# Kernel optimization log

Hardware: AMD Instinct MI355X
Metric: run time of the kernel (lower is better)

## Reference

```python
import jax
import jax.numpy as jnp
from jax import lax
import numpy as np

L, B, D_IN, D = 1024, 16, 2048, 2048
K = 3  # n_in == n_out -> k = 3, highway uses x directly


def setup_inputs() -> dict:
    key = jax.random.key(0)
    k1, k2 = jax.random.split(key)
    x = jax.random.normal(k1, (L, B, D_IN), dtype=jnp.float32)
    c0 = jnp.zeros((B, D), dtype=jnp.float32)
    # learned params: projection weight (n_in, n_out*k) and bias (2*n_out)
    weight = jax.random.normal(k2, (D_IN, D * K), dtype=jnp.float32) * (1.0 / np.sqrt(D_IN))
    bias = jnp.zeros((2 * D,), dtype=jnp.float32)
    return {"x": x, "c0": c0, "weight": weight, "bias": bias}


def reference(x, c0, weight, bias):
    # x: [L, B, n_in], c0: [B, d], weight: [n_in, d*3], bias: [2*d]
    Llen, Bsz, _ = x.shape
    d = c0.shape[-1]
    u = jnp.einsum("lbi,ik->lbk", x, weight).reshape(Llen, Bsz, d, K)
    u0 = u[..., 0]                                   # candidate
    g1 = jax.nn.sigmoid(u[..., 1] + bias[:d])        # forget gate
    g2 = jax.nn.sigmoid(u[..., 2] + bias[d:])        # highway/reset gate

    # sequential recurrence: c_t = (c_{t-1} - u0_t) * g1_t + u0_t
    def step(c_prev, inp):
        u0_t, g1_t = inp
        c_t = (c_prev - u0_t) * g1_t + u0_t
        return c_t, c_t

    c_last, cs = lax.scan(step, c0, (u0, g1))
    # h_t = (tanh(c_t) - x_t) * g2_t + x_t   (use_tanh=1, k=3 highway on x)
    h = (jnp.tanh(cs) - x) * g2 + x
    return h, c_last
```

## Files before the change

### kernel.cpp

```cpp
#include <hip/hip_runtime.h>
#include <hip/hip_bf16.h>
#include <cstdint>

#define L_SEQ 1024
#define BSZ   16
#define DIN   2048
#define DD    2048
#define MROWS (L_SEQ * BSZ)
#define NCOLS (3 * DD)
#define BKT   64
#define NT    (DIN / BKT)

typedef __attribute__((ext_vector_type(8))) short  short8;
typedef __attribute__((ext_vector_type(4))) float  f32x4;
typedef __attribute__((ext_vector_type(4))) ushort ushort4v;

typedef const __attribute__((address_space(1))) void* gas_ptr;
typedef __attribute__((address_space(3))) void*       las_ptr;

#define GLOAD16(g, l) __builtin_amdgcn_global_load_lds((gas_ptr)(g), (las_ptr)(l), 16, 0, 0)

__device__ __forceinline__ float bf2f(ushort u) {
    return __uint_as_float(((uint32_t)u) << 16);
}
__device__ __forceinline__ ushort f2bf(float f) {
    uint32_t u = __float_as_uint(f);
    uint32_t r = u + 0x7FFFu + ((u >> 16) & 1u);
    return (ushort)(r >> 16);
}

__global__ __launch_bounds__(256) void cvt_x_kernel(const f32x4* __restrict__ x,
                                                    ushort4v* __restrict__ xb, int n4) {
    int i = blockIdx.x * blockDim.x + threadIdx.x;
    int stride = gridDim.x * blockDim.x;
    for (; i < n4; i += stride) {
        f32x4 v = x[i];
        ushort4v o;
        o.x = f2bf(v.x); o.y = f2bf(v.y); o.z = f2bf(v.z); o.w = f2bf(v.w);
        xb[i] = o;
    }
}

__global__ __launch_bounds__(256) void transpose_w_kernel(const float* __restrict__ W,
                                                          ushort* __restrict__ WT) {
    __shared__ float tile[64][65];
    int k0 = blockIdx.x * 64;
    int n0 = blockIdx.y * 64;
    int c  = threadIdx.x & 63;
    int r0 = threadIdx.x >> 6;
#pragma unroll
    for (int rr = 0; rr < 16; ++rr) {
        int r = r0 + rr * 4;
        tile[r][c] = W[(size_t)(k0 + r) * NCOLS + n0 + c];
    }
    __syncthreads();
#pragma unroll
    for (int rr = 0; rr < 16; ++rr) {
        int r = r0 + rr * 4;
        int n = n0 + r;
        int nprime = (n % 3) * DD + (n / 3);
        WT[(size_t)nprime * DIN + k0 + c] = f2bf(tile[c][r]);
    }
}

#define SLOT(b, s) (&lds8[(((b) << 2) + (s)) * 8192])

#define STAGE_A(b, h, kt) do {                                                   \
    const ushort* _g = Ab + (size_t)((h) * 64 + idx) * DIN + (kt) * BKT + akc;   \
    ushort* _l = SLOT(b, (h)) + tid * 8;                                         \
    GLOAD16(_g, _l);                                                             \
    GLOAD16(_g + (size_t)128 * DIN, _l + 4096);                                  \
} while (0)

#define STAGE_B(b, h2, kt) do {                                                  \
    const ushort* _g0 = Bb + (size_t)(brow0 + (h2) * 32) * DIN + (kt) * BKT + akc;\
    const ushort* _g1 = Bb + (size_t)(brow1 + (h2) * 32) * DIN + (kt) * BKT + akc;\
    ushort* _l = SLOT(b, 2 + (h2)) + tid * 8;                                    \
    GLOAD16(_g0, _l);                                                            \
    GLOAD16(_g1, _l + 4096);                                                     \
} while (0)

#define LD_A(b, h) do { const ushort* _s = SLOT(b, (h)) + a_rb;                  \
    _Pragma("unroll") for (int _m = 0; _m < 4; ++_m) {                           \
        aF[_m][0] = *(const short8*)(_s + _m * 1024 + cs0);                      \
        aF[_m][1] = *(const short8*)(_s + _m * 1024 + cs1); }                    \
} while (0)

#define LD_B(b, h2, bF) do { const ushort* _s = SLOT(b, 2 + (h2)) + b_rb;        \
    _Pragma("unroll") for (int _n = 0; _n < 2; ++_n) {                           \
        bF[_n][0] = *(const short8*)(_s + _n * 1024 + cs0);                      \
        bF[_n][1] = *(const short8*)(_s + _n * 1024 + cs1); }                    \
} while (0)

#define MM(mb, bF, nb) do {                                                      \
    __builtin_amdgcn_s_setprio(1);                                               \
    _Pragma("unroll") for (int _m = 0; _m < 4; ++_m)                             \
    _Pragma("unroll") for (int _n = 0; _n < 2; ++_n) {                           \
        acc[(mb)+_m][(nb)+_n] = __builtin_amdgcn_mfma_f32_16x16x32_bf16(         \
            aF[_m][0], bF[_n][0], acc[(mb)+_m][(nb)+_n], 0, 0, 0);               \
        acc[(mb)+_m][(nb)+_n] = __builtin_amdgcn_mfma_f32_16x16x32_bf16(         \
            aF[_m][1], bF[_n][1], acc[(mb)+_m][(nb)+_n], 0, 0, 0); }             \
    __builtin_amdgcn_s_setprio(0);                                               \
    __builtin_amdgcn_sched_barrier(0);                                           \
} while (0)

#define BAR() __builtin_amdgcn_s_barrier()

__global__ __launch_bounds__(512, 2) void sru_gemm8(const ushort* __restrict__ A,
                                                    const ushort* __restrict__ Bt,
                                                    const float*  __restrict__ bias,
                                                    ushort* __restrict__ u0,
                                                    ushort* __restrict__ g1,
                                                    ushort* __restrict__ g2) {
    __shared__ alignas(16) ushort lds8[65536];

    int bid = blockIdx.x;
    int swz = (bid & 7) * 192 + (bid >> 3);
    int bm0 = (swz / 24) * 256;
    int bn0 = (swz % 24) * 256;

    int tid  = threadIdx.x;
    int wave = tid >> 6, lane = tid & 63;
    int wm = wave >> 2, wn = wave & 3;

    int idx    = tid >> 3;
    int schunk = (tid & 7) ^ (idx & 7);
    int akc    = schunk * 8;
    int brow0  = (idx >> 5) * 64 + (idx & 31);
    int brow1  = ((idx >> 5) + 2) * 64 + (idx & 31);
    const ushort* Ab = A  + (size_t)bm0 * DIN;
    const ushort* Bb = Bt + (size_t)bn0 * DIN;

    int lrow = lane & 15, lk = lane >> 4, lx = lane & 7;
    int cs0  = ((0 + lk) ^ lx) * 8;
    int cs1  = ((4 + lk) ^ lx) * 8;
    int a_rb = (wm * 64 + lrow) * 64;
    int b_rb = (wn * 32 + lrow) * 64;

    f32x4 acc[8][4];
    f32x4 zero = {0.f, 0.f, 0.f, 0.f};
#pragma unroll
    for (int i = 0; i < 8; ++i)
#pragma unroll
        for (int j = 0; j < 4; ++j) acc[i][j] = zero;

    STAGE_A(0, 0, 0); STAGE_A(0, 1, 0); STAGE_B(0, 0, 0); STAGE_B(0, 1, 0);
    STAGE_A(1, 0, 1); STAGE_B(1, 0, 1);
    asm volatile("s_waitcnt vmcnt(4)" ::: "memory");
    BAR();

    short8 aF[4][2], bF0[2][2], bF1[2][2];

    for (int t = 0; t < NT; ++t) {
        int cur = t & 1, nxt = cur ^ 1;
        int kt1 = (t + 1 < NT) ? t + 1 : NT - 1;
        int kt2 = (t + 2 < NT) ? t + 2 : NT - 1;
        LD_A(cur, 0); LD_B(cur, 0, bF0);
        STAGE_A(nxt, 1, kt1);
        BAR(); MM(0, bF0, 0); BAR();
        LD_B(cur, 1, bF1);
        STAGE_B(nxt, 1, kt1);
        BAR(); MM(0, bF1, 2); BAR();
        LD_A(cur, 1);
        STAGE_A(cur, 0, kt2);
        BAR(); MM(4, bF0, 0); BAR();
        STAGE_B(cur, 0, kt2);
        asm volatile("s_waitcnt vmcnt(4)" ::: "memory");
        BAR(); MM(4, bF1, 2); BAR();
    }
    asm volatile("s_waitcnt vmcnt(0)" ::: "memory");

    int region = bn0 >> 11;
    int col_l  = (bn0 & (DD - 1)) + wn * 64 + (lane & 15);
#pragma unroll
    for (int mf = 0; mf < 8; ++mf) {
        int rowb = bm0 + wm * 128 + mf * 16 + ((lane >> 4) << 2);
#pragma unroll
        for (int nf = 0; nf < 4; ++nf) {
            int col = col_l + nf * 16;
#pragma unroll
            for (int r = 0; r < 4; ++r) {
                float v = acc[mf][nf][r];
                size_t o = (size_t)(rowb + r) * DD + col;
                if (region == 0) {
                    u0[o] = f2bf(v);
                } else {
                    float z = v + bias[(region - 1) * DD + col];
                    float g = 1.f / (1.f + __expf(-z));
                    (region == 1 ? g1 : g2)[o] = f2bf(g);
                }
            }
        }
    }
}

__global__ __launch_bounds__(64) void sru_rec(const ushort* __restrict__ u0,
                                              const ushort* __restrict__ g1,
                                              const ushort* __restrict__ g2,
                                              const float*  __restrict__ x,
                                              const float*  __restrict__ c0,
                                              float* __restrict__ h,
                                              float* __restrict__ c_last) {
    int t = blockIdx.x * 64 + threadIdx.x;
    float c = c0[t];
#pragma unroll 8
    for (int l = 0; l < L_SEQ; ++l) {
        int ix = l * (BSZ * DD) + t;
        float uu  = bf2f(u0[ix]);
        float gg1 = bf2f(g1[ix]);
        float gg2 = bf2f(g2[ix]);
        float xx  = x[ix];
        c = (c - uu) * gg1 + uu;
        float e  = __expf(-2.f * fabsf(c));
        float th = (1.f - e) / (1.f + e);
        th = copysignf(th, c);
        h[ix] = (th - xx) * gg2 + xx;
    }
    c_last[t] = c;
}

extern "C" void kernel_launch(void* const* d_in, const int* in_sizes, int n_in,
                              void* d_out, int out_size, void* d_ws, size_t ws_size,
                              hipStream_t stream) {
    const float* x    = (const float*)d_in[0];
    const float* c0   = (const float*)d_in[1];
    const float* W    = (const float*)d_in[2];
    const float* bias = (const float*)d_in[3];
    float* out = (float*)d_out;

    char* ws = (char*)d_ws;
    ushort* xb = (ushort*)(ws);
    ushort* WT = (ushort*)(ws + 67108864);
    ushort* u0 = (ushort*)(ws + 92274688);
    ushort* g1 = (ushort*)(ws + 159383552);
    ushort* g2 = (ushort*)(ws + 226492416);

    hipLaunchKernelGGL(cvt_x_kernel, dim3(2048), dim3(256), 0, stream,
                       (const f32x4*)x, (ushort4v*)xb, MROWS * DIN / 4);
    hipLaunchKernelGGL(transpose_w_kernel, dim3(32, 96), dim3(256), 0, stream, W, WT);
    hipLaunchKernelGGL(sru_gemm8, dim3(1536), dim3(512), 0, stream, xb, WT, bias, u0, g1, g2);
    hipLaunchKernelGGL(sru_rec, dim3(512), dim3(64), 0, stream,
                       u0, g1, g2, x, c0, out, out + (size_t)MROWS * DD);
}
```

Before: 630.2 us.

## Transpose MFMA output layout for packed bf16 epilogue stores and read bf16 x

Swaps the MFMA operand order so each lane's accumulator holds four consecutive columns instead of four rows. The epilogue can then pack values with v_cvt_pk_bf16_f32 and write 8-byte stores rather than scattered 2-byte ones, and the bias is loaded as a float4. The recurrence kernel now reads the bf16 copy of x instead of the fp32 input, which halves that stream's traffic. The cost is that the highway term uses x rounded to bf16, so h loses some precision.

```diff
diff --git a/kernel.cpp b/kernel.cpp
--- a/kernel.cpp
+++ b/kernel.cpp
@@ -97,9 +97,9 @@
     _Pragma("unroll") for (int _m = 0; _m < 4; ++_m)                             \
     _Pragma("unroll") for (int _n = 0; _n < 2; ++_n) {                           \
         acc[(mb)+_m][(nb)+_n] = __builtin_amdgcn_mfma_f32_16x16x32_bf16(         \
-            aF[_m][0], bF[_n][0], acc[(mb)+_m][(nb)+_n], 0, 0, 0);               \
+            bF[_n][0], aF[_m][0], acc[(mb)+_m][(nb)+_n], 0, 0, 0);               \
         acc[(mb)+_m][(nb)+_n] = __builtin_amdgcn_mfma_f32_16x16x32_bf16(         \
-            aF[_m][1], bF[_n][1], acc[(mb)+_m][(nb)+_n], 0, 0, 0); }             \
+            bF[_n][1], aF[_m][1], acc[(mb)+_m][(nb)+_n], 0, 0, 0); }             \
     __builtin_amdgcn_s_setprio(0);                                               \
     __builtin_amdgcn_sched_barrier(0);                                           \
 } while (0)
@@ -171,24 +171,44 @@
     asm volatile("s_waitcnt vmcnt(0)" ::: "memory");
 
     int region = bn0 >> 11;
-    int col_l  = (bn0 & (DD - 1)) + wn * 64 + (lane & 15);
-#pragma unroll
-    for (int mf = 0; mf < 8; ++mf) {
-        int rowb = bm0 + wm * 128 + mf * 16 + ((lane >> 4) << 2);
-#pragma unroll
-        for (int nf = 0; nf < 4; ++nf) {
-            int col = col_l + nf * 16;
-#pragma unroll
-            for (int r = 0; r < 4; ++r) {
-                float v = acc[mf][nf][r];
-                size_t o = (size_t)(rowb + r) * DD + col;
-                if (region == 0) {
-                    u0[o] = f2bf(v);
-                } else {
-                    float z = v + bias[(region - 1) * DD + col];
-                    float g = 1.f / (1.f + __expf(-z));
-                    (region == 1 ? g1 : g2)[o] = f2bf(g);
-                }
+    int colb = (bn0 & (DD - 1)) + wn * 64 + ((lane >> 4) << 2);
+    int rowm = bm0 + wm * 128 + (lane & 15);
+    if (region == 0) {
+#pragma unroll
+        for (int j = 0; j < 4; ++j)
+#pragma unroll
+            for (int i = 0; i < 4; ++i) {
+                f32x4 v = acc[i][j];
+                uint32_t lo, hi;
+                asm("v_cvt_pk_bf16_f32 %0, %1, %2" : "=v"(lo) : "v"(v[0]), "v"(v[1]));
+                asm("v_cvt_pk_bf16_f32 %0, %1, %2" : "=v"(hi) : "v"(v[2]), "v"(v[3]));
+                uint2 pk; pk.x = lo; pk.y = hi;
+                *(uint2*)&u0[(size_t)(rowm + i * 16) * DD + colb + j * 16] = pk;
+                f32x4 w = acc[4 + i][j];
+                asm("v_cvt_pk_bf16_f32 %0, %1, %2" : "=v"(lo) : "v"(w[0]), "v"(w[1]));
+                asm("v_cvt_pk_bf16_f32 %0, %1, %2" : "=v"(hi) : "v"(w[2]), "v"(w[3]));
+                pk.x = lo; pk.y = hi;
+                *(uint2*)&u0[(size_t)(rowm + 64 + i * 16) * DD + colb + j * 16] = pk;
+            }
+    } else {
+        const float* bp = bias + (size_t)(region - 1) * DD;
+        ushort* gp = (region == 1) ? g1 : g2;
+#pragma unroll
+        for (int j = 0; j < 4; ++j) {
+            float4 bv = *(const float4*)&bp[colb + j * 16];
+#pragma unroll
+            for (int i = 0; i < 8; ++i) {
+                f32x4 v = acc[i][j];
+                float s0 = 1.f / (1.f + __expf(-(v[0] + bv.x)));
+                float s1 = 1.f / (1.f + __expf(-(v[1] + bv.y)));
+                float s2 = 1.f / (1.f + __expf(-(v[2] + bv.z)));
+                float s3 = 1.f / (1.f + __expf(-(v[3] + bv.w)));
+                uint32_t lo, hi;
+                asm("v_cvt_pk_bf16_f32 %0, %1, %2" : "=v"(lo) : "v"(s0), "v"(s1));
+                asm("v_cvt_pk_bf16_f32 %0, %1, %2" : "=v"(hi) : "v"(s2), "v"(s3));
+                uint2 pk; pk.x = lo; pk.y = hi;
+                int rr = rowm + (i >> 2) * 64 + (i & 3) * 16;
+                *(uint2*)&gp[(size_t)rr * DD + colb + j * 16] = pk;
             }
         }
     }
@@ -197,7 +217,7 @@
 __global__ __launch_bounds__(64) void sru_rec(const ushort* __restrict__ u0,
                                               const ushort* __restrict__ g1,
                                               const ushort* __restrict__ g2,
-                                              const float*  __restrict__ x,
+                                              const ushort* __restrict__ xb,
                                               const float*  __restrict__ c0,
                                               float* __restrict__ h,
                                               float* __restrict__ c_last) {
@@ -209,7 +229,7 @@
         float uu  = bf2f(u0[ix]);
         float gg1 = bf2f(g1[ix]);
         float gg2 = bf2f(g2[ix]);
-        float xx  = x[ix];
+        float xx  = bf2f(xb[ix]);
         c = (c - uu) * gg1 + uu;
         float e  = __expf(-2.f * fabsf(c));
         float th = (1.f - e) / (1.f + e);
@@ -240,5 +260,5 @@
     hipLaunchKernelGGL(transpose_w_kernel, dim3(32, 96), dim3(256), 0, stream, W, WT);
     hipLaunchKernelGGL(sru_gemm8, dim3(1536), dim3(512), 0, stream, xb, WT, bias, u0, g1, g2);
     hipLaunchKernelGGL(sru_rec, dim3(512), dim3(64), 0, stream,
-                       u0, g1, g2, x, c0, out, out + (size_t)MROWS * DD);
-}
+                       u0, g1, g2, xb, c0, out, out + (size_t)MROWS * DD);
+}
```

New measurement: 583.5 us. 7.4% less time.
